# Kernel tuning notes

Measured on AMD Instinct MI355X. Metric: run time of the kernel, lower is better.

The kernel has to match this reference:

```python
import jax, jax.numpy as jnp
import numpy as np

HIDDEN = 2048
HEAD_DIM = 128
Q_HEAD = 16
KV_HEAD = 2
MAX_TOKEN = 4096
THETA = 10000
B = 1
S = 2048
SCALER = 1.0 / np.sqrt(HEAD_DIM)


def make_pos_emb():
    # Faithful port of ROPEEmbedding.create_embedding
    i = np.repeat(np.arange(HEAD_DIM // 2), 2)            # [D]
    freq = np.power(float(THETA), -i * 2.0 / HEAD_DIM)    # [D]
    t = np.einsum('i,j->ij', freq, np.arange(MAX_TOKEN, dtype=np.float64))  # [D, T]
    cos = np.cos(t)
    sin = np.sin(t)
    sin[0::2] *= -1.0                                      # negate even rows (even dim indices)
    pe = np.concatenate([cos, sin], axis=0).T              # [T, 2D]
    return jnp.asarray(pe, jnp.float32)


def _flip_pairs(x):
    # swap adjacent pairs along last dim: (x0,x1,x2,x3,..) -> (x1,x0,x3,x2,..)
    b, h, s, d = x.shape
    return x.reshape(b, h, s, d // 2, 2)[..., ::-1].reshape(b, h, s, d)


def _apply_rope(x, pos_emb):
    # x: [B, H, S, D]; pos_emb: [max_token, 2D]
    s = x.shape[2]
    pe = pos_emb[:s]                     # [S, 2D]
    cos = pe[:, :HEAD_DIM]               # [S, D]
    sin = pe[:, HEAD_DIM:]               # [S, D] (signed)
    return x * cos + _flip_pairs(x) * sin


def setup_inputs() -> dict:
    key = jax.random.key(0)
    ks = jax.random.split(key, 5)
    qkv_out = (Q_HEAD + 2 * KV_HEAD) * HEAD_DIM  # 2560
    lim_qkv = 1.0 / np.sqrt(HIDDEN)
    lim_o = 1.0 / np.sqrt(Q_HEAD * HEAD_DIM)
    x = jax.random.normal(ks[0], (B, S, HIDDEN), dtype=jnp.float32)
    w_qkv = jax.random.uniform(ks[1], (qkv_out, HIDDEN), jnp.float32, -lim_qkv, lim_qkv)
    b_qkv = jax.random.uniform(ks[2], (qkv_out,), jnp.float32, -lim_qkv, lim_qkv)
    w_o = jax.random.uniform(ks[3], (HIDDEN, Q_HEAD * HEAD_DIM), jnp.float32, -lim_o, lim_o)
    b_o = jax.random.uniform(ks[4], (HIDDEN,), jnp.float32, -lim_o, lim_o)
    # causal additive mask, as typically passed to this module
    neg = jnp.float32(-1e9)
    attention_mask = jnp.where(
        jnp.tril(jnp.ones((S, S), dtype=bool)), jnp.float32(0.0), neg
    )[None, None, :, :]
    pos_emb = make_pos_emb()
    return {"tensor": x, "attention_mask": attention_mask, "w_qkv": w_qkv,
            "b_qkv": b_qkv, "w_o": w_o, "b_o": b_o, "pos_emb": pos_emb}


def reference(tensor, attention_mask, w_qkv, b_qkv, w_o, b_o, pos_emb):
    b, s, _ = tensor.shape
    qkv = tensor @ w_qkv.T + b_qkv                        # [B, S, 2560]
    dq = HEAD_DIM * Q_HEAD
    dkv = HEAD_DIM * KV_HEAD
    q = qkv[..., :dq].reshape(b, s, Q_HEAD, HEAD_DIM)
    k = qkv[..., dq:dq + dkv].reshape(b, s, KV_HEAD, HEAD_DIM)
    v = qkv[..., dq + dkv:].reshape(b, s, KV_HEAD, HEAD_DIM)
    scale = Q_HEAD // KV_HEAD
    k = jnp.repeat(k, scale, axis=2)                      # [B, S, Q_HEAD, D]
    v = jnp.repeat(v, scale, axis=2)
    q = q.transpose(0, 2, 1, 3)                           # [B, H, S, D]
    k = k.transpose(0, 2, 1, 3)
    v = v.transpose(0, 2, 1, 3)
    q = _apply_rope(q, pos_emb)
    k = _apply_rope(k, pos_emb)
    scores = jnp.einsum('bhqd,bhkd->bhqk', q, k) * SCALER
    scores = scores + attention_mask
    attn = jax.nn.softmax(scores, axis=-1)
    out = jnp.einsum('bhqk,bhkd->bhqd', attn, v)          # [B, H, S, D]
    out = out.transpose(0, 2, 1, 3).reshape(b, s, Q_HEAD * HEAD_DIM)
    return out @ w_o.T + b_o
```

## Files before the change

kernel.cpp:

```cpp
#include <hip/hip_runtime.h>
#include <stdint.h>

#define SQ 2048
#define DH 128
#define SCALER 0.08838834764831845f

typedef float f32x4 __attribute__((ext_vector_type(4)));
typedef short s16x8 __attribute__((ext_vector_type(8)));
typedef short s16x4 __attribute__((ext_vector_type(4)));

__device__ __forceinline__ short f2bf(float f) {
  uint32_t x = __float_as_uint(f);
  uint32_t r = (x + 0x7fffu + ((x >> 16) & 1u)) >> 16;
  return (short)(r & 0xffffu);
}

__device__ __forceinline__ void mfma16(f32x4& d, s16x8 a, s16x8 b) {
  asm("v_mfma_f32_16x16x32_bf16 %0, %1, %2, %0" : "+v"(d) : "v"(a), "v"(b));
}

__device__ __forceinline__ void gload16(const void* g, void* l) {
  __builtin_amdgcn_global_load_lds(
      (__attribute__((address_space(1))) void*)const_cast<void*>(g),
      (__attribute__((address_space(3))) void*)l, 16, 0, 0);
}

__global__ __launch_bounds__(256) void cvt3_bf16(
    const float* __restrict__ a, const float* __restrict__ b,
    const float* __restrict__ c, short* __restrict__ out,
    int na8, int nb8, int nc8) {
  int i = blockIdx.x * 256 + threadIdx.x;
  if (i >= na8 + nb8 + nc8) return;
  const float* src;
  if (i < na8) src = a + (size_t)i * 8;
  else if (i < na8 + nb8) src = b + (size_t)(i - na8) * 8;
  else src = c + (size_t)(i - na8 - nb8) * 8;
  const float4* p = (const float4*)src;
  float4 u = p[0], v = p[1];
  s16x8 o;
  o[0] = f2bf(u.x); o[1] = f2bf(u.y); o[2] = f2bf(u.z); o[3] = f2bf(u.w);
  o[4] = f2bf(v.x); o[5] = f2bf(v.y); o[6] = f2bf(v.z); o[7] = f2bf(v.w);
  *((s16x8*)out + i) = o;
}

template <int MODE>
__global__ __launch_bounds__(256) void gemm_bt_bias(
    const short* __restrict__ A, const short* __restrict__ B,
    const float* __restrict__ bias, float* __restrict__ C,
    const float* __restrict__ pe, short* __restrict__ qws,
    short* __restrict__ kws, short* __restrict__ vtws,
    int M, int N, int K) {
  __shared__ __align__(16) short smem[128 * 64 + 64 * 64];
  short* As = smem;
  short* Bs = smem + 128 * 64;
  const int t = threadIdx.x;
  const int l = t & 63, w = t >> 6;
  const int wr = w >> 1, wc = w & 1;
  const int lr = l & 15, lk = l >> 4;
  const int m0 = blockIdx.y * 128, n0 = blockIdx.x * 64;

  f32x4 acc[4][2] = {};

  for (int kt = 0; kt < K; kt += 64) {
    const short* ga = A + (size_t)m0 * K + kt;
    const short* gb = B + (size_t)n0 * K + kt;
#pragma unroll
    for (int i = 0; i < 4; ++i) {
      int j = i * 256 + t;
      int lbase = (i * 256 + (t & ~63)) << 4;
      gload16(ga + (size_t)(j >> 3) * K + ((j & 7) << 3), (char*)As + lbase);
    }
#pragma unroll
    for (int i = 0; i < 2; ++i) {
      int j = i * 256 + t;
      int lbase = (i * 256 + (t & ~63)) << 4;
      gload16(gb + (size_t)(j >> 3) * K + ((j & 7) << 3), (char*)Bs + lbase);
    }
    __syncthreads();
#pragma unroll
    for (int ks = 0; ks < 2; ++ks) {
      s16x8 af[4], bg[2];
#pragma unroll
      for (int i = 0; i < 4; ++i)
        af[i] = *(const s16x8*)(As + (wr * 64 + i * 16 + lr) * 64 + ks * 32 + lk * 8);
#pragma unroll
      for (int i = 0; i < 2; ++i)
        bg[i] = *(const s16x8*)(Bs + (wc * 32 + i * 16 + lr) * 64 + ks * 32 + lk * 8);
#pragma unroll
      for (int mi = 0; mi < 4; ++mi)
#pragma unroll
        for (int ni = 0; ni < 2; ++ni)
          mfma16(acc[mi][ni], af[mi], bg[ni]);
    }
    __syncthreads();
  }

  if (MODE == 0) {
#pragma unroll
    for (int mi = 0; mi < 4; ++mi) {
      int row = m0 + wr * 64 + mi * 16 + lk * 4;
#pragma unroll
      for (int ni = 0; ni < 2; ++ni) {
        int col = n0 + wc * 32 + ni * 16 + lr;
        float bv = bias[col];
#pragma unroll
        for (int r = 0; r < 4; ++r)
          C[(size_t)(row + r) * N + col] = acc[mi][ni][r] + bv;
      }
    }
  } else {
    if (n0 < 2304) {
      short* Ct = smem;
#pragma unroll
      for (int mi = 0; mi < 4; ++mi) {
        int row_l = wr * 64 + mi * 16 + lk * 4;
#pragma unroll
        for (int ni = 0; ni < 2; ++ni) {
          int col_l = wc * 32 + ni * 16 + lr;
          int col = n0 + col_l;
          float bv = bias[col];
          int d = col & 127;
#pragma unroll
          for (int r = 0; r < 4; ++r) {
            float v = acc[mi][ni][r] + bv;
            float p = __shfl_xor(v, 1);
            int s = m0 + row_l + r;
            const float* per = pe + (size_t)s * 256;
            float y = v * per[d] + p * per[128 + d];
            if (n0 < 2048) y *= SCALER;
            Ct[(row_l + r) * 72 + col_l] = f2bf(y);
          }
        }
      }
      __syncthreads();
      if (n0 < 2048) {
        int hq = n0 >> 7, d0 = n0 & 127;
#pragma unroll
        for (int i = 0; i < 4; ++i) {
          int idx = i * 256 + t;
          int sl = idx >> 3, c = idx & 7;
          s16x8 val = *(const s16x8*)(Ct + sl * 72 + c * 8);
          *(s16x8*)(qws + ((size_t)hq * SQ + m0 + sl) * DH + d0 + c * 8) = val;
        }
      } else {
        int hk = (n0 - 2048) >> 7, d0 = (n0 - 2048) & 127;
#pragma unroll
        for (int i = 0; i < 4; ++i) {
          int idx = i * 256 + t;
          int sl = idx >> 3, c = idx & 7;
          s16x8 val = *(const s16x8*)(Ct + sl * 72 + c * 8);
          int slot = ((d0 >> 3) + c) ^ (sl & 15);
          *(s16x8*)(kws + (size_t)hk * SQ * DH + (size_t)(m0 + sl) * DH + slot * 8) = val;
        }
      }
    } else {
      short* Ct = smem;
      int hk = (n0 - 2304) >> 7, d0 = (n0 - 2304) & 127;
#pragma unroll
      for (int mi = 0; mi < 4; ++mi) {
        int row_l = wr * 64 + mi * 16 + lk * 4;
#pragma unroll
        for (int ni = 0; ni < 2; ++ni) {
          int col_l = wc * 32 + ni * 16 + lr;
          float bv = bias[n0 + col_l];
#pragma unroll
          for (int r = 0; r < 4; ++r)
            Ct[col_l * 136 + row_l + r] = f2bf(acc[mi][ni][r] + bv);
        }
      }
      __syncthreads();
#pragma unroll
      for (int i = 0; i < 4; ++i) {
        int idx = i * 256 + t;
        int dl = idx >> 4, c = idx & 15;
        s16x8 val = *(const s16x8*)(Ct + dl * 136 + c * 8);
        int d = d0 + dl;
        size_t dst = (size_t)hk * DH * SQ + (size_t)d * SQ +
                     (size_t)((m0 >> 6) + (c >> 3)) * 64 +
                     (size_t)(((c & 7) ^ (d & 7)) << 3);
        *(s16x8*)(vtws + dst) = val;
      }
    }
  }
}

__global__ __launch_bounds__(256) void attn_fwd(
    const short* __restrict__ qws, const short* __restrict__ kws,
    const short* __restrict__ vtws, short* __restrict__ attnws) {
  __shared__ __align__(16) short Ks[2][64 * 128];
  __shared__ __align__(16) short Vt[2][128 * 64];
  __shared__ __align__(16) short Ps[4][16 * 72];

  const int bx = blockIdx.x;
  const int h = bx & 15;
  const int i_ = bx >> 4;
  const int qb = (i_ < 16) ? (31 - i_) : (i_ - 16);
  const int hk = h >> 3;
  const int t = threadIdx.x, l = t & 63, w = t >> 6;
  const int lr = l & 15, lk = l >> 4;

  s16x8 qf[4];
  {
    const short* qbase = qws + ((size_t)h * SQ + (size_t)qb * 64 + w * 16) * DH;
#pragma unroll
    for (int kd = 0; kd < 4; ++kd)
      qf[kd] = *(const s16x8*)(qbase + (size_t)lr * DH + kd * 32 + lk * 8);
  }

  f32x4 o[8] = {};
  float m_ = -1e30f, l_ = 0.f;

  const short* gkh = kws + (size_t)hk * SQ * DH;
  const short* gvh = vtws + (size_t)hk * DH * SQ;

#define STAGE(buf, kb)                                                          \
  {                                                                             \
    const short* gk = gkh + (size_t)(kb)*64 * DH;                               \
    const short* gv = gvh + (size_t)(kb)*64;                                    \
    _Pragma("unroll") for (int i = 0; i < 4; ++i) {                             \
      int j = i * 256 + t;                                                      \
      int lbase = (i * 256 + (t & ~63)) << 4;                                   \
      gload16(gk + (size_t)(j >> 4) * DH + ((j & 15) << 3),                     \
              (char*)Ks[buf] + lbase);                                          \
      gload16(gv + (size_t)(j >> 3) * SQ + ((j & 7) << 3),                      \
              (char*)Vt[buf] + lbase);                                          \
    }                                                                           \
  }

  STAGE(0, 0);
  __syncthreads();

  for (int kb = 0; kb <= qb; ++kb) {
    const int cur = kb & 1;
    if (kb < qb) STAGE(cur ^ 1, kb + 1);

    f32x4 sc_[4] = {};
#pragma unroll
    for (int kd = 0; kd < 4; ++kd) {
#pragma unroll
      for (int nt = 0; nt < 4; ++nt) {
        int krow = nt * 16 + lr;
        int slot = (kd * 4 + lk) ^ lr;
        s16x8 kf = *(const s16x8*)(Ks[cur] + krow * 128 + slot * 8);
        mfma16(sc_[nt], kf, qf[kd]);
      }
    }
    if (kb == qb) {
      int qloc = w * 16 + lr;
#pragma unroll
      for (int nt = 0; nt < 4; ++nt)
#pragma unroll
        for (int r = 0; r < 4; ++r) {
          int col = nt * 16 + lk * 4 + r;
          if (col > qloc) sc_[nt][r] = -1e30f;
        }
    }
    {
      float rm = -1e30f;
#pragma unroll
      for (int nt = 0; nt < 4; ++nt)
        rm = fmaxf(rm, fmaxf(fmaxf(sc_[nt][0], sc_[nt][1]),
                             fmaxf(sc_[nt][2], sc_[nt][3])));
      rm = fmaxf(rm, __shfl_xor(rm, 16));
      rm = fmaxf(rm, __shfl_xor(rm, 32));
      float mn = fmaxf(m_, rm);
      float scl = __expf(m_ - mn);
      float rs = 0.f;
#pragma unroll
      for (int nt = 0; nt < 4; ++nt)
#pragma unroll
        for (int r = 0; r < 4; ++r) {
          sc_[nt][r] = __expf(sc_[nt][r] - mn);
          rs += sc_[nt][r];
        }
      rs += __shfl_xor(rs, 16);
      rs += __shfl_xor(rs, 32);
      l_ = l_ * scl + rs;
      m_ = mn;
#pragma unroll
      for (int dt = 0; dt < 8; ++dt)
#pragma unroll
        for (int r = 0; r < 4; ++r) o[dt][r] *= scl;
    }
    {
      short* ps = (short*)Ps[w];
#pragma unroll
      for (int nt = 0; nt < 4; ++nt)
#pragma unroll
        for (int r = 0; r < 4; ++r)
          ps[lr * 72 + nt * 16 + lk * 4 + r] = f2bf(sc_[nt][r]);
    }
    {
      const short* ps = (const short*)Ps[w];
#pragma unroll
      for (int kp = 0; kp < 2; ++kp) {
        s16x8 pbf = *(const s16x8*)(ps + lr * 72 + kp * 32 + lk * 8);
#pragma unroll
        for (int dt = 0; dt < 8; ++dt) {
          int drow = dt * 16 + lr;
          int slot = (kp * 4 + lk) ^ (lr & 7);
          s16x8 vb = *(const s16x8*)(Vt[cur] + drow * 64 + slot * 8);
          mfma16(o[dt], vb, pbf);
        }
      }
    }
    __syncthreads();
  }
#undef STAGE

  {
    int srow = qb * 64 + w * 16 + lr;
#pragma unroll
    for (int dt = 0; dt < 8; ++dt) {
      s16x4 st;
#pragma unroll
      for (int r = 0; r < 4; ++r) st[r] = f2bf(o[dt][r] / l_);
      *(s16x4*)(attnws + (size_t)srow * 2048 + h * DH + dt * 16 + lk * 4) = st;
    }
  }
}

extern "C" void kernel_launch(void* const* d_in, const int* in_sizes, int n_in,
                              void* d_out, int out_size, void* d_ws, size_t ws_size,
                              hipStream_t stream) {
  (void)in_sizes; (void)n_in; (void)out_size; (void)ws_size;
  const float* x     = (const float*)d_in[0];
  const float* w_qkv = (const float*)d_in[2];
  const float* b_qkv = (const float*)d_in[3];
  const float* w_o   = (const float*)d_in[4];
  const float* b_o   = (const float*)d_in[5];
  const float* pe    = (const float*)d_in[6];
  float* out = (float*)d_out;

  short* xb     = (short*)d_ws;
  short* wqkvb  = xb + (size_t)2048 * 2048;
  short* wob    = wqkvb + (size_t)2560 * 2048;
  short* qws    = wob + (size_t)2048 * 2048;
  short* kws    = qws + (size_t)16 * 2048 * 128;
  short* vtws   = kws + (size_t)2 * 2048 * 128;
  short* attnws = vtws + (size_t)2 * 128 * 2048;

  cvt3_bf16<<<6656, 256, 0, stream>>>(x, w_qkv, w_o, xb,
                                      2048 * 2048 / 8, 2560 * 2048 / 8, 2048 * 2048 / 8);
  gemm_bt_bias<1><<<dim3(2560 / 64, 2048 / 128), 256, 0, stream>>>(
      xb, wqkvb, b_qkv, nullptr, pe, qws, kws, vtws, 2048, 2560, 2048);
  attn_fwd<<<512, 256, 0, stream>>>(qws, kws, vtws, attnws);
  gemm_bt_bias<0><<<dim3(2048 / 64, 2048 / 128), 256, 0, stream>>>(
      attnws, wob, b_o, out, nullptr, nullptr, nullptr, nullptr, 2048, 2048, 2048);
}
```

Before: 149.6 us.

## Process two 16-row query tiles per wave in attention, halving block threads

The attention kernel now runs two waves per block instead of four, and each wave handles 32 query rows as two 16-row MFMA tiles. Each K fragment and V fragment read from LDS is reused for two MFMAs, which halves LDS traffic per MFMA. In exchange, per-thread register use roughly doubles (two output accumulators, two score tiles), there are fewer waves to hide latency, and each thread issues twice as many staging loads.

```diff
diff --git a/kernel.cpp b/kernel.cpp
--- a/kernel.cpp
+++ b/kernel.cpp
@@ -184,12 +184,12 @@
   }
 }
 
-__global__ __launch_bounds__(256) void attn_fwd(
+__global__ __launch_bounds__(128) void attn_fwd(
     const short* __restrict__ qws, const short* __restrict__ kws,
     const short* __restrict__ vtws, short* __restrict__ attnws) {
   __shared__ __align__(16) short Ks[2][64 * 128];
   __shared__ __align__(16) short Vt[2][128 * 64];
-  __shared__ __align__(16) short Ps[4][16 * 72];
+  __shared__ __align__(16) short Ps[2][32 * 72];
 
   const int bx = blockIdx.x;
   const int h = bx & 15;
@@ -199,16 +199,18 @@
   const int t = threadIdx.x, l = t & 63, w = t >> 6;
   const int lr = l & 15, lk = l >> 4;
 
-  s16x8 qf[4];
+  s16x8 qf[2][4];
   {
-    const short* qbase = qws + ((size_t)h * SQ + (size_t)qb * 64 + w * 16) * DH;
-#pragma unroll
-    for (int kd = 0; kd < 4; ++kd)
-      qf[kd] = *(const s16x8*)(qbase + (size_t)lr * DH + kd * 32 + lk * 8);
-  }
-
-  f32x4 o[8] = {};
-  float m_ = -1e30f, l_ = 0.f;
+    const short* qbase = qws + ((size_t)h * SQ + (size_t)qb * 64 + w * 32) * DH;
+#pragma unroll
+    for (int qt = 0; qt < 2; ++qt)
+#pragma unroll
+      for (int kd = 0; kd < 4; ++kd)
+        qf[qt][kd] = *(const s16x8*)(qbase + (size_t)(qt * 16 + lr) * DH + kd * 32 + lk * 8);
+  }
+
+  f32x4 o[2][8] = {};
+  float m_[2] = {-1e30f, -1e30f}, l_[2] = {0.f, 0.f};
 
   const short* gkh = kws + (size_t)hk * SQ * DH;
   const short* gvh = vtws + (size_t)hk * DH * SQ;
@@ -217,9 +219,9 @@
   {                                                                             \
     const short* gk = gkh + (size_t)(kb)*64 * DH;                               \
     const short* gv = gvh + (size_t)(kb)*64;                                    \
-    _Pragma("unroll") for (int i = 0; i < 4; ++i) {                             \
-      int j = i * 256 + t;                                                      \
-      int lbase = (i * 256 + (t & ~63)) << 4;                                   \
+    _Pragma("unroll") for (int i = 0; i < 8; ++i) {                             \
+      int j = i * 128 + t;                                                      \
+      int lbase = (i * 128 + (t & ~63)) << 4;                                   \
       gload16(gk + (size_t)(j >> 4) * DH + ((j & 15) << 3),                     \
               (char*)Ks[buf] + lbase);                                          \
       gload16(gv + (size_t)(j >> 3) * SQ + ((j & 7) << 3),                      \
@@ -234,7 +236,7 @@
     const int cur = kb & 1;
     if (kb < qb) STAGE(cur ^ 1, kb + 1);
 
-    f32x4 sc_[4] = {};
+    f32x4 sc_[2][4] = {};
 #pragma unroll
     for (int kd = 0; kd < 4; ++kd) {
 #pragma unroll
@@ -242,65 +244,70 @@
         int krow = nt * 16 + lr;
         int slot = (kd * 4 + lk) ^ lr;
         s16x8 kf = *(const s16x8*)(Ks[cur] + krow * 128 + slot * 8);
-        mfma16(sc_[nt], kf, qf[kd]);
+        mfma16(sc_[0][nt], kf, qf[0][kd]);
+        mfma16(sc_[1][nt], kf, qf[1][kd]);
       }
     }
     if (kb == qb) {
-      int qloc = w * 16 + lr;
+#pragma unroll
+      for (int qt = 0; qt < 2; ++qt) {
+        int qloc = w * 32 + qt * 16 + lr;
+#pragma unroll
+        for (int nt = 0; nt < 4; ++nt)
+#pragma unroll
+          for (int r = 0; r < 4; ++r) {
+            int col = nt * 16 + lk * 4 + r;
+            if (col > qloc) sc_[qt][nt][r] = -1e30f;
+          }
+      }
+    }
+#pragma unroll
+    for (int qt = 0; qt < 2; ++qt) {
+      float rm = -1e30f;
 #pragma unroll
       for (int nt = 0; nt < 4; ++nt)
-#pragma unroll
-        for (int r = 0; r < 4; ++r) {
-          int col = nt * 16 + lk * 4 + r;
-          if (col > qloc) sc_[nt][r] = -1e30f;
-        }
-    }
-    {
-      float rm = -1e30f;
-#pragma unroll
-      for (int nt = 0; nt < 4; ++nt)
-        rm = fmaxf(rm, fmaxf(fmaxf(sc_[nt][0], sc_[nt][1]),
-                             fmaxf(sc_[nt][2], sc_[nt][3])));
+        rm = fmaxf(rm, fmaxf(fmaxf(sc_[qt][nt][0], sc_[qt][nt][1]),
+                             fmaxf(sc_[qt][nt][2], sc_[qt][nt][3])));
       rm = fmaxf(rm, __shfl_xor(rm, 16));
       rm = fmaxf(rm, __shfl_xor(rm, 32));
-      float mn = fmaxf(m_, rm);
-      float scl = __expf(m_ - mn);
+      float mn = fmaxf(m_[qt], rm);
+      float scl = __expf(m_[qt] - mn);
       float rs = 0.f;
 #pragma unroll
       for (int nt = 0; nt < 4; ++nt)
 #pragma unroll
         for (int r = 0; r < 4; ++r) {
-          sc_[nt][r] = __expf(sc_[nt][r] - mn);
-          rs += sc_[nt][r];
+          sc_[qt][nt][r] = __expf(sc_[qt][nt][r] - mn);
+          rs += sc_[qt][nt][r];
         }
       rs += __shfl_xor(rs, 16);
       rs += __shfl_xor(rs, 32);
-      l_ = l_ * scl + rs;
-      m_ = mn;
+      l_[qt] = l_[qt] * scl + rs;
+      m_[qt] = mn;
 #pragma unroll
       for (int dt = 0; dt < 8; ++dt)
 #pragma unroll
-        for (int r = 0; r < 4; ++r) o[dt][r] *= scl;
-    }
-    {
+        for (int r = 0; r < 4; ++r) o[qt][dt][r] *= scl;
       short* ps = (short*)Ps[w];
 #pragma unroll
       for (int nt = 0; nt < 4; ++nt)
 #pragma unroll
         for (int r = 0; r < 4; ++r)
-          ps[lr * 72 + nt * 16 + lk * 4 + r] = f2bf(sc_[nt][r]);
+          ps[(qt * 16 + lr) * 72 + nt * 16 + lk * 4 + r] = f2bf(sc_[qt][nt][r]);
     }
     {
       const short* ps = (const short*)Ps[w];
 #pragma unroll
       for (int kp = 0; kp < 2; ++kp) {
-        s16x8 pbf = *(const s16x8*)(ps + lr * 72 + kp * 32 + lk * 8);
+        s16x8 pb0 = *(const s16x8*)(ps + lr * 72 + kp * 32 + lk * 8);
+        s16x8 pb1 = *(const s16x8*)(ps + (16 + lr) * 72 + kp * 32 + lk * 8);
 #pragma unroll
         for (int dt = 0; dt < 8; ++dt) {
           int drow = dt * 16 + lr;
           int slot = (kp * 4 + lk) ^ (lr & 7);
           s16x8 vb = *(const s16x8*)(Vt[cur] + drow * 64 + slot * 8);
-          mfma16(o[dt], vb, pbf);
+          mfma16(o[0][dt], vb, pb0);
+          mfma16(o[1][dt], vb, pb1);
         }
       }
     }
@@ -308,13 +315,14 @@
   }
 #undef STAGE
 
-  {
-    int srow = qb * 64 + w * 16 + lr;
+#pragma unroll
+  for (int qt = 0; qt < 2; ++qt) {
+    int srow = qb * 64 + w * 32 + qt * 16 + lr;
 #pragma unroll
     for (int dt = 0; dt < 8; ++dt) {
       s16x4 st;
 #pragma unroll
-      for (int r = 0; r < 4; ++r) st[r] = f2bf(o[dt][r] / l_);
+      for (int r = 0; r < 4; ++r) st[r] = f2bf(o[qt][dt][r] / l_[qt]);
       *(s16x4*)(attnws + (size_t)srow * 2048 + h * DH + dt * 16 + lk * 4) = st;
     }
   }
@@ -344,7 +352,7 @@
                                       2048 * 2048 / 8, 2560 * 2048 / 8, 2048 * 2048 / 8);
   gemm_bt_bias<1><<<dim3(2560 / 64, 2048 / 128), 256, 0, stream>>>(
       xb, wqkvb, b_qkv, nullptr, pe, qws, kws, vtws, 2048, 2560, 2048);
-  attn_fwd<<<512, 256, 0, stream>>>(qws, kws, vtws, attnws);
+  attn_fwd<<<512, 128, 0, stream>>>(qws, kws, vtws, attnws);
   gemm_bt_bias<0><<<dim3(2048 / 64, 2048 / 128), 256, 0, stream>>>(
       attnws, wob, b_o, out, nullptr, nullptr, nullptr, nullptr, 2048, 2048, 2048);
 }
```

New measurement: 166.1 us. 1.11x slower.
